# Optimization experiments

Measured on AMD Instinct MI355X. Metric: run time of the kernel, lower is better.

The kernel has to match this reference:

```python
import jax, jax.numpy as jnp
import numpy as np

EMBED_DIM = 768
NUM_HEADS = 12
HEAD_DIM = EMBED_DIM // NUM_HEADS


def setup_inputs() -> dict:
    key = jax.random.key(0)
    ks = jax.random.split(key, 5)
    B, N, D = 8, 1024, EMBED_DIM
    s = 1.0 / np.sqrt(D)
    return {
        "x": jax.random.normal(ks[0], (B, N, D), dtype=jnp.float32),
        "qkv_w": jax.random.uniform(ks[1], (D, 3 * D), jnp.float32, -s, s),  # [in, out]
        "qkv_b": jax.random.uniform(ks[2], (3 * D,), jnp.float32, -s, s),
        "proj_w": jax.random.uniform(ks[3], (D, D), jnp.float32, -s, s),
        "proj_b": jax.random.uniform(ks[4], (D,), jnp.float32, -s, s),
    }


def reference(x, qkv_w, qkv_b, proj_w, proj_b):
    B, N, D = x.shape
    H, Hd = NUM_HEADS, HEAD_DIM
    qkv = x @ qkv_w + qkv_b                          # [B, N, 3D]
    qkv = qkv.reshape(B, N, 3, H, Hd)
    q, k, v = (jnp.moveaxis(qkv, 2, 0)[i].transpose(0, 2, 1, 3) for i in range(3))  # each [B, H, N, Hd]
    scores = jnp.einsum("bhnd,bhmd->bhnm", q, k) / np.sqrt(Hd).astype(x.dtype)
    attn = jax.nn.softmax(scores, axis=-1)           # dropout rate 0.0 -> identity
    out = jnp.einsum("bhnm,bhmd->bhnd", attn, v)     # [B, H, N, Hd]
    out = out.transpose(0, 2, 1, 3).reshape(B, N, D)
    return out @ proj_w + proj_b
```

## Files before the change

### kernel.cpp

```cpp
#include <hip/hip_runtime.h>
#include <hip/hip_bf16.h>

typedef __attribute__((ext_vector_type(8))) short short8;
typedef __attribute__((ext_vector_type(4))) float f32x4;
typedef __attribute__((ext_vector_type(2))) unsigned int uint2v;
typedef unsigned int u32;

__device__ inline ushort f2bf(float f) {
    unsigned int i = __builtin_bit_cast(unsigned int, f);
    unsigned int r = (i + 0x7FFFu + ((i >> 16) & 1u)) >> 16;
    return (ushort)r;
}
__device__ inline u32 pack_bf16(float a, float b) {
    return (u32)f2bf(a) | ((u32)f2bf(b) << 16);
}

__device__ __forceinline__ void gload_lds16(const ushort* g, ushort* l) {
    __builtin_amdgcn_global_load_lds(
        (const __attribute__((address_space(1))) u32*)g,
        (__attribute__((address_space(3))) u32*)l, 16, 0, 0);
}

__global__ __launch_bounds__(256) void convert_f32_bf16(
    const float* __restrict__ in, ushort* __restrict__ outp, int n8)
{
    int idx = blockIdx.x * 256 + threadIdx.x;
    if (idx >= n8) return;
    const float4 u0 = *(const float4*)&in[(size_t)idx * 8];
    const float4 u1 = *(const float4*)&in[(size_t)idx * 8 + 4];
    short8 v;
    v[0] = (short)f2bf(u0.x); v[1] = (short)f2bf(u0.y);
    v[2] = (short)f2bf(u0.z); v[3] = (short)f2bf(u0.w);
    v[4] = (short)f2bf(u1.x); v[5] = (short)f2bf(u1.y);
    v[6] = (short)f2bf(u1.z); v[7] = (short)f2bf(u1.w);
    *(short8*)&outp[(size_t)idx * 8] = v;
}

__global__ __launch_bounds__(256) void transpose_f32_bf16(
    const float* __restrict__ W, ushort* __restrict__ Wt, int K, int N)
{
    __shared__ float tile[32][33];
    const int n0 = blockIdx.x * 32;
    const int k0 = blockIdx.y * 32;
    const int tx = threadIdx.x & 31;
    const int ty = threadIdx.x >> 5;
    for (int i = ty; i < 32; i += 8)
        tile[i][tx] = W[(size_t)(k0 + i) * N + n0 + tx];
    __syncthreads();
    for (int i = ty; i < 32; i += 8)
        Wt[(size_t)(n0 + i) * K + k0 + tx] = f2bf(tile[tx][i]);
}

template <bool OUT_FP32, bool QKV_MODE>
__global__ __launch_bounds__(256) void gemm_bt(
    const ushort* __restrict__ A, const ushort* __restrict__ Bt,
    const float* __restrict__ bias, void* __restrict__ C,
    ushort* __restrict__ Vt, int M, int N, int K, int ldc)
{
    __shared__ __attribute__((aligned(16))) ushort As[128][64];
    __shared__ __attribute__((aligned(16))) ushort Bs[128][64];
    const int tid  = threadIdx.x;
    const int lane = tid & 63;
    const int w    = tid >> 6;
    const int wm   = (w >> 1) * 64;
    const int wn   = (w & 1) * 64;
    const int g    = lane >> 4;
    const int t    = lane & 15;
    const int m0   = blockIdx.y * 128;
    const int n0   = blockIdx.x * 128;

    const int lr = lane >> 3;
    const int pc = lane & 7;

    f32x4 acc[4][4];
#pragma unroll
    for (int i = 0; i < 4; i++)
#pragma unroll
        for (int j = 0; j < 4; j++) acc[i][j] = {0.f, 0.f, 0.f, 0.f};

    const int xorc = t & 7;

    for (int k0 = 0; k0 < K; k0 += 64) {
#pragma unroll
        for (int p = 0; p < 4; p++) {
            const int row = w * 32 + p * 8 + lr;
            const int gc  = pc ^ (row & 7);
            gload_lds16(&A[(size_t)(m0 + row) * K + k0 + gc * 8], &As[w * 32 + p * 8][0]);
            gload_lds16(&Bt[(size_t)(n0 + row) * K + k0 + gc * 8], &Bs[w * 32 + p * 8][0]);
        }
        __syncthreads();
#pragma unroll
        for (int s = 0; s < 2; s++) {
            short8 a[4], b[4];
            const int ca = ((s * 4 + g) ^ xorc) * 8;
#pragma unroll
            for (int i = 0; i < 4; i++)
                a[i] = *(const short8*)&As[wm + i * 16 + t][ca];
#pragma unroll
            for (int j = 0; j < 4; j++)
                b[j] = *(const short8*)&Bs[wn + j * 16 + t][ca];
#pragma unroll
            for (int i = 0; i < 4; i++)
#pragma unroll
                for (int j = 0; j < 4; j++)
                    acc[i][j] = __builtin_amdgcn_mfma_f32_16x16x32_bf16(
                        a[i], b[j], acc[i][j], 0, 0, 0);
        }
        __syncthreads();
    }

#pragma unroll
    for (int j = 0; j < 4; j++) {
        int col = n0 + wn + j * 16 + t;
        float bv = bias[col];
        if (QKV_MODE && col >= 1536) {
            int h = (col - 1536) >> 6, d = col & 63;
#pragma unroll
            for (int i = 0; i < 4; i++) {
                int n = m0 + wm + i * 16 + g * 4;
                int bb = n >> 10, nn = n & 1023;
                uint2v u;
                u.x = pack_bf16(acc[i][j][0] + bv, acc[i][j][1] + bv);
                u.y = pack_bf16(acc[i][j][2] + bv, acc[i][j][3] + bv);
                *(uint2v*)&Vt[(((size_t)bb * 12 + h) * 64 + d) * 1024 + nn] = u;
            }
        } else {
#pragma unroll
            for (int i = 0; i < 4; i++)
#pragma unroll
                for (int r = 0; r < 4; r++) {
                    int row = m0 + wm + i * 16 + g * 4 + r;
                    float val = acc[i][j][r] + bv;
                    if (OUT_FP32) ((float*)C)[(size_t)row * ldc + col] = val;
                    else          ((ushort*)C)[(size_t)row * ldc + col] = f2bf(val);
                }
        }
    }
}

#define SD 72
__global__ __launch_bounds__(256) void attn_kernel(
    const ushort* __restrict__ qk, const ushort* __restrict__ Vt,
    ushort* __restrict__ out)
{
    __shared__ __attribute__((aligned(16))) ushort Ks[2][64][SD];
    __shared__ __attribute__((aligned(16))) ushort Vs[2][64][SD];
    __shared__ __attribute__((aligned(16))) ushort Ps[4][16][SD];

    const int tid  = threadIdx.x;
    const int lane = tid & 63;
    const int w    = tid >> 6;
    const int g    = lane >> 4;
    const int t    = lane & 15;
    const int q0   = blockIdx.x * 64;
    const int h    = blockIdx.y;
    const int b    = blockIdx.z;

    const int srow = tid >> 3;
    const int scol = (tid & 7) * 8;
    const size_t base  = (size_t)b * 1024 * 1536;
    const size_t vbase = ((size_t)b * 12 + h) * 64 * 1024;
    const float SC = 0.125f * 1.44269504088896f;

    short8 qfrag[2];
#pragma unroll
    for (int s = 0; s < 2; s++)
        qfrag[s] = *(const short8*)&qk[base + (size_t)(q0 + w * 16 + t) * 1536 +
                                       h * 64 + s * 32 + g * 8];

#pragma unroll
    for (int p = 0; p < 2; p++) {
        int r = srow + 32 * p;
        *(short8*)&Ks[0][r][scol] =
            *(const short8*)&qk[base + (size_t)r * 1536 + 768 + h * 64 + scol];
        *(short8*)&Vs[0][r][scol] =
            *(const short8*)&Vt[vbase + (size_t)r * 1024 + scol];
    }
    __syncthreads();

    f32x4 o_acc[4];
#pragma unroll
    for (int j = 0; j < 4; j++) o_acc[j] = {0.f, 0.f, 0.f, 0.f};
    float l_part = 0.f;

    for (int kt = 0; kt < 16; kt++) {
        const int cur = kt & 1;

        short8 kpre[2], vpre[2];
        if (kt < 15) {
            const int kb = (kt + 1) * 64;
#pragma unroll
            for (int p = 0; p < 2; p++) {
                int r = srow + 32 * p;
                kpre[p] = *(const short8*)&qk[base + (size_t)(kb + r) * 1536 + 768 + h * 64 + scol];
                vpre[p] = *(const short8*)&Vt[vbase + (size_t)r * 1024 + kb + scol];
            }
        }

        f32x4 s_acc[4];
#pragma unroll
        for (int j = 0; j < 4; j++) s_acc[j] = {0.f, 0.f, 0.f, 0.f};
#pragma unroll
        for (int s = 0; s < 2; s++)
#pragma unroll
            for (int j = 0; j < 4; j++) {
                short8 kf = *(const short8*)&Ks[cur][j * 16 + t][s * 32 + g * 8];
                s_acc[j] = __builtin_amdgcn_mfma_f32_16x16x32_bf16(kf, qfrag[s], s_acc[j], 0, 0, 0);
            }

#pragma unroll
        for (int j = 0; j < 4; j++) {
            float p0 = exp2f(s_acc[j][0] * SC);
            float p1 = exp2f(s_acc[j][1] * SC);
            float p2 = exp2f(s_acc[j][2] * SC);
            float p3 = exp2f(s_acc[j][3] * SC);
            l_part += (p0 + p1) + (p2 + p3);
            uint2v u;
            u.x = pack_bf16(p0, p1);
            u.y = pack_bf16(p2, p3);
            *(uint2v*)&Ps[w][t][j * 16 + g * 4] = u;
        }

#pragma unroll
        for (int s = 0; s < 2; s++) {
            short8 a = *(const short8*)&Ps[w][t][s * 32 + g * 8];
#pragma unroll
            for (int j = 0; j < 4; j++) {
                short8 bv = *(const short8*)&Vs[cur][j * 16 + t][s * 32 + g * 8];
                o_acc[j] = __builtin_amdgcn_mfma_f32_16x16x32_bf16(a, bv, o_acc[j], 0, 0, 0);
            }
        }

        if (kt < 15) {
#pragma unroll
            for (int p = 0; p < 2; p++) {
                int r = srow + 32 * p;
                *(short8*)&Ks[cur ^ 1][r][scol] = kpre[p];
                *(short8*)&Vs[cur ^ 1][r][scol] = vpre[p];
            }
        }
        __syncthreads();
    }

    float l_tot = l_part;
    l_tot += __shfl_xor(l_tot, 16);
    l_tot += __shfl_xor(l_tot, 32);
    float il[4];
#pragma unroll
    for (int r = 0; r < 4; r++) il[r] = 1.0f / __shfl(l_tot, g * 4 + r);
#pragma unroll
    for (int r = 0; r < 4; r++) {
        int row = q0 + w * 16 + g * 4 + r;
#pragma unroll
        for (int j = 0; j < 4; j++)
            out[((size_t)(b * 1024 + row)) * 768 + h * 64 + j * 16 + t] =
                f2bf(o_acc[j][r] * il[r]);
    }
}

extern "C" void kernel_launch(void* const* d_in, const int* in_sizes, int n_in,
                              void* d_out, int out_size, void* d_ws, size_t ws_size,
                              hipStream_t stream)
{
    const float* x      = (const float*)d_in[0];
    const float* qkv_w  = (const float*)d_in[1];
    const float* qkv_b  = (const float*)d_in[2];
    const float* proj_w = (const float*)d_in[3];
    const float* proj_b = (const float*)d_in[4];
    float* out = (float*)d_out;

    char* ws = (char*)d_ws;
    ushort* Wt1 = (ushort*)ws;
    ushort* Wt2 = Wt1 + (size_t)2304 * 768;
    char*   buf = (char*)(Wt2 + (size_t)768 * 768);

    transpose_f32_bf16<<<dim3(72, 24), 256, 0, stream>>>(qkv_w, Wt1, 768, 2304);
    transpose_f32_bf16<<<dim3(24, 24), 256, 0, stream>>>(proj_w, Wt2, 768, 768);

    const size_t wt_bytes   = ((size_t)2304 * 768 + (size_t)768 * 768) * 2;
    const size_t full_bytes = wt_bytes + (size_t)8192 * 768 * 2
                                       + (size_t)8192 * 1536 * 2
                                       + (size_t)8192 * 768 * 2
                                       + (size_t)8192 * 768 * 2;

    if (ws_size >= full_bytes) {
        ushort* xb    = (ushort*)buf;
        ushort* qkO   = xb + (size_t)8192 * 768;
        ushort* VtO   = qkO + (size_t)8192 * 1536;
        ushort* attnO = VtO + (size_t)8192 * 768;
        convert_f32_bf16<<<dim3(3072), 256, 0, stream>>>(x, xb, 786432);
        gemm_bt<false, true><<<dim3(18, 64), 256, 0, stream>>>(
            xb, Wt1, qkv_b, qkO, VtO, 8192, 2304, 768, 1536);
        attn_kernel<<<dim3(16, 12, 8), 256, 0, stream>>>(qkO, VtO, attnO);
        gemm_bt<true, false><<<dim3(6, 64), 256, 0, stream>>>(
            attnO, Wt2, proj_b, out, nullptr, 8192, 768, 768, 768);
    } else {
        ushort* xbB   = (ushort*)buf;
        ushort* qkB   = xbB + (size_t)1024 * 768;
        ushort* VtB   = qkB + (size_t)1024 * 1536;
        ushort* attnB = VtB + (size_t)1024 * 768;
        for (int b = 0; b < 8; b++) {
            const float* xp = x + (size_t)b * 1024 * 768;
            float* outb = out + (size_t)b * 1024 * 768;
            convert_f32_bf16<<<dim3(384), 256, 0, stream>>>(xp, xbB, 98304);
            gemm_bt<false, true><<<dim3(18, 8), 256, 0, stream>>>(
                xbB, Wt1, qkv_b, qkB, VtB, 1024, 2304, 768, 1536);
            attn_kernel<<<dim3(16, 12, 1), 256, 0, stream>>>(qkB, VtB, attnB);
            gemm_bt<true, false><<<dim3(6, 8), 256, 0, stream>>>(
                attnB, Wt2, proj_b, outb, nullptr, 1024, 768, 768, 768);
        }
    }
}
```

Before: 221.3 us.

## Process 128 queries per attention block with swizzled K/V LDS and prescaled Q

```diff
diff --git a/kernel.cpp b/kernel.cpp
--- a/kernel.cpp
+++ b/kernel.cpp
@@ -6,13 +6,18 @@
 typedef __attribute__((ext_vector_type(2))) unsigned int uint2v;
 typedef unsigned int u32;
 
+#define QSCALE 0.1803368801111204f
+
 __device__ inline ushort f2bf(float f) {
     unsigned int i = __builtin_bit_cast(unsigned int, f);
     unsigned int r = (i + 0x7FFFu + ((i >> 16) & 1u)) >> 16;
     return (ushort)r;
 }
 __device__ inline u32 pack_bf16(float a, float b) {
-    return (u32)f2bf(a) | ((u32)f2bf(b) << 16);
+    float2 f2; f2.x = a; f2.y = b;
+    __hip_bfloat162 h = __float22bfloat162_rn(f2);
+    u32 r; __builtin_memcpy(&r, &h, 4);
+    return r;
 }
 
 __device__ __forceinline__ void gload_lds16(const ushort* g, ushort* l) {
@@ -28,12 +33,11 @@
     if (idx >= n8) return;
     const float4 u0 = *(const float4*)&in[(size_t)idx * 8];
     const float4 u1 = *(const float4*)&in[(size_t)idx * 8 + 4];
-    short8 v;
-    v[0] = (short)f2bf(u0.x); v[1] = (short)f2bf(u0.y);
-    v[2] = (short)f2bf(u0.z); v[3] = (short)f2bf(u0.w);
-    v[4] = (short)f2bf(u1.x); v[5] = (short)f2bf(u1.y);
-    v[6] = (short)f2bf(u1.z); v[7] = (short)f2bf(u1.w);
-    *(short8*)&outp[(size_t)idx * 8] = v;
+    uint2v a, b;
+    a.x = pack_bf16(u0.x, u0.y); a.y = pack_bf16(u0.z, u0.w);
+    b.x = pack_bf16(u1.x, u1.y); b.y = pack_bf16(u1.z, u1.w);
+    *(uint2v*)&outp[(size_t)idx * 8] = a;
+    *(uint2v*)&outp[(size_t)idx * 8 + 4] = b;
 }
 
 __global__ __launch_bounds__(256) void transpose_f32_bf16(
@@ -131,6 +135,7 @@
                 for (int r = 0; r < 4; r++) {
                     int row = m0 + wm + i * 16 + g * 4 + r;
                     float val = acc[i][j][r] + bv;
+                    if (QKV_MODE && col < 768) val *= QSCALE;
                     if (OUT_FP32) ((float*)C)[(size_t)row * ldc + col] = val;
                     else          ((ushort*)C)[(size_t)row * ldc + col] = f2bf(val);
                 }
@@ -138,50 +143,54 @@
     }
 }
 
-#define SD 72
+#define PD 72
 __global__ __launch_bounds__(256) void attn_kernel(
     const ushort* __restrict__ qk, const ushort* __restrict__ Vt,
     ushort* __restrict__ out)
 {
-    __shared__ __attribute__((aligned(16))) ushort Ks[2][64][SD];
-    __shared__ __attribute__((aligned(16))) ushort Vs[2][64][SD];
-    __shared__ __attribute__((aligned(16))) ushort Ps[4][16][SD];
+    __shared__ __attribute__((aligned(16))) ushort Ks[2][64][64];
+    __shared__ __attribute__((aligned(16))) ushort Vs[2][64][64];
+    __shared__ __attribute__((aligned(16))) ushort Ps[4][16][PD];
 
     const int tid  = threadIdx.x;
     const int lane = tid & 63;
     const int w    = tid >> 6;
     const int g    = lane >> 4;
     const int t    = lane & 15;
-    const int q0   = blockIdx.x * 64;
+    const int q0   = blockIdx.x * 128;
     const int h    = blockIdx.y;
     const int b    = blockIdx.z;
 
     const int srow = tid >> 3;
-    const int scol = (tid & 7) * 8;
+    const int pc   = tid & 7;
     const size_t base  = (size_t)b * 1024 * 1536;
     const size_t vbase = ((size_t)b * 12 + h) * 64 * 1024;
-    const float SC = 0.125f * 1.44269504088896f;
-
-    short8 qfrag[2];
-#pragma unroll
-    for (int s = 0; s < 2; s++)
-        qfrag[s] = *(const short8*)&qk[base + (size_t)(q0 + w * 16 + t) * 1536 +
-                                       h * 64 + s * 32 + g * 8];
+
+    short8 qfrag[2][2];
+#pragma unroll
+    for (int qf = 0; qf < 2; qf++)
+#pragma unroll
+        for (int s = 0; s < 2; s++)
+            qfrag[qf][s] = *(const short8*)&qk[base +
+                (size_t)(q0 + qf * 64 + w * 16 + t) * 1536 + h * 64 + s * 32 + g * 8];
 
 #pragma unroll
     for (int p = 0; p < 2; p++) {
         int r = srow + 32 * p;
-        *(short8*)&Ks[0][r][scol] =
-            *(const short8*)&qk[base + (size_t)r * 1536 + 768 + h * 64 + scol];
-        *(short8*)&Vs[0][r][scol] =
-            *(const short8*)&Vt[vbase + (size_t)r * 1024 + scol];
+        int c = (pc ^ (r & 7)) * 8;
+        *(short8*)&Ks[0][r][c] =
+            *(const short8*)&qk[base + (size_t)r * 1536 + 768 + h * 64 + pc * 8];
+        *(short8*)&Vs[0][r][c] =
+            *(const short8*)&Vt[vbase + (size_t)r * 1024 + pc * 8];
     }
     __syncthreads();
 
-    f32x4 o_acc[4];
-#pragma unroll
-    for (int j = 0; j < 4; j++) o_acc[j] = {0.f, 0.f, 0.f, 0.f};
-    float l_part = 0.f;
+    f32x4 o_acc[2][4];
+#pragma unroll
+    for (int qf = 0; qf < 2; qf++)
+#pragma unroll
+        for (int j = 0; j < 4; j++) o_acc[qf][j] = {0.f, 0.f, 0.f, 0.f};
+    float l_part[2] = {0.f, 0.f};
 
     for (int kt = 0; kt < 16; kt++) {
         const int cur = kt & 1;
@@ -192,42 +201,54 @@
 #pragma unroll
             for (int p = 0; p < 2; p++) {
                 int r = srow + 32 * p;
-                kpre[p] = *(const short8*)&qk[base + (size_t)(kb + r) * 1536 + 768 + h * 64 + scol];
-                vpre[p] = *(const short8*)&Vt[vbase + (size_t)r * 1024 + kb + scol];
-            }
-        }
-
-        f32x4 s_acc[4];
-#pragma unroll
-        for (int j = 0; j < 4; j++) s_acc[j] = {0.f, 0.f, 0.f, 0.f};
+                kpre[p] = *(const short8*)&qk[base + (size_t)(kb + r) * 1536 + 768 + h * 64 + pc * 8];
+                vpre[p] = *(const short8*)&Vt[vbase + (size_t)r * 1024 + kb + pc * 8];
+            }
+        }
+
+        short8 kf[2][4], bv[2][4];
 #pragma unroll
         for (int s = 0; s < 2; s++)
 #pragma unroll
             for (int j = 0; j < 4; j++) {
-                short8 kf = *(const short8*)&Ks[cur][j * 16 + t][s * 32 + g * 8];
-                s_acc[j] = __builtin_amdgcn_mfma_f32_16x16x32_bf16(kf, qfrag[s], s_acc[j], 0, 0, 0);
-            }
-
-#pragma unroll
-        for (int j = 0; j < 4; j++) {
-            float p0 = exp2f(s_acc[j][0] * SC);
-            float p1 = exp2f(s_acc[j][1] * SC);
-            float p2 = exp2f(s_acc[j][2] * SC);
-            float p3 = exp2f(s_acc[j][3] * SC);
-            l_part += (p0 + p1) + (p2 + p3);
-            uint2v u;
-            u.x = pack_bf16(p0, p1);
-            u.y = pack_bf16(p2, p3);
-            *(uint2v*)&Ps[w][t][j * 16 + g * 4] = u;
-        }
-
-#pragma unroll
-        for (int s = 0; s < 2; s++) {
-            short8 a = *(const short8*)&Ps[w][t][s * 32 + g * 8];
+                const int row = j * 16 + t;
+                const int c = ((s * 4 + g) ^ (t & 7)) * 8;
+                kf[s][j] = *(const short8*)&Ks[cur][row][c];
+                bv[s][j] = *(const short8*)&Vs[cur][row][c];
+            }
+
+#pragma unroll
+        for (int qf = 0; qf < 2; qf++) {
+            f32x4 s_acc[4];
+#pragma unroll
+            for (int j = 0; j < 4; j++) s_acc[j] = {0.f, 0.f, 0.f, 0.f};
+#pragma unroll
+            for (int s = 0; s < 2; s++)
+#pragma unroll
+                for (int j = 0; j < 4; j++)
+                    s_acc[j] = __builtin_amdgcn_mfma_f32_16x16x32_bf16(
+                        kf[s][j], qfrag[qf][s], s_acc[j], 0, 0, 0);
+
 #pragma unroll
             for (int j = 0; j < 4; j++) {
-                short8 bv = *(const short8*)&Vs[cur][j * 16 + t][s * 32 + g * 8];
-                o_acc[j] = __builtin_amdgcn_mfma_f32_16x16x32_bf16(a, bv, o_acc[j], 0, 0, 0);
+                float p0 = exp2f(s_acc[j][0]);
+                float p1 = exp2f(s_acc[j][1]);
+                float p2 = exp2f(s_acc[j][2]);
+                float p3 = exp2f(s_acc[j][3]);
+                l_part[qf] += (p0 + p1) + (p2 + p3);
+                uint2v u;
+                u.x = pack_bf16(p0, p1);
+                u.y = pack_bf16(p2, p3);
+                *(uint2v*)&Ps[w][t][j * 16 + g * 4] = u;
+            }
+
+#pragma unroll
+            for (int s = 0; s < 2; s++) {
+                short8 a = *(const short8*)&Ps[w][t][s * 32 + g * 8];
+#pragma unroll
+                for (int j = 0; j < 4; j++)
+                    o_acc[qf][j] = __builtin_amdgcn_mfma_f32_16x16x32_bf16(
+                        a, bv[s][j], o_acc[qf][j], 0, 0, 0);
             }
         }
 
@@ -235,26 +256,30 @@
 #pragma unroll
             for (int p = 0; p < 2; p++) {
                 int r = srow + 32 * p;
-                *(short8*)&Ks[cur ^ 1][r][scol] = kpre[p];
-                *(short8*)&Vs[cur ^ 1][r][scol] = vpre[p];
+                int c = (pc ^ (r & 7)) * 8;
+                *(short8*)&Ks[cur ^ 1][r][c] = kpre[p];
+                *(short8*)&Vs[cur ^ 1][r][c] = vpre[p];
             }
         }
         __syncthreads();
     }
 
-    float l_tot = l_part;
-    l_tot += __shfl_xor(l_tot, 16);
-    l_tot += __shfl_xor(l_tot, 32);
-    float il[4];
-#pragma unroll
-    for (int r = 0; r < 4; r++) il[r] = 1.0f / __shfl(l_tot, g * 4 + r);
-#pragma unroll
-    for (int r = 0; r < 4; r++) {
-        int row = q0 + w * 16 + g * 4 + r;
-#pragma unroll
-        for (int j = 0; j < 4; j++)
-            out[((size_t)(b * 1024 + row)) * 768 + h * 64 + j * 16 + t] =
-                f2bf(o_acc[j][r] * il[r]);
+#pragma unroll
+    for (int qf = 0; qf < 2; qf++) {
+        float l_tot = l_part[qf];
+        l_tot += __shfl_xor(l_tot, 16);
+        l_tot += __shfl_xor(l_tot, 32);
+        float il[4];
+#pragma unroll
+        for (int r = 0; r < 4; r++) il[r] = 1.0f / __shfl(l_tot, g * 4 + r);
+#pragma unroll
+        for (int r = 0; r < 4; r++) {
+            int row = q0 + qf * 64 + w * 16 + g * 4 + r;
+#pragma unroll
+            for (int j = 0; j < 4; j++)
+                out[((size_t)(b * 1024 + row)) * 768 + h * 64 + j * 16 + t] =
+                    f2bf(o_acc[qf][j][r] * il[r]);
+        }
     }
 }
 
@@ -291,7 +316,7 @@
         convert_f32_bf16<<<dim3(3072), 256, 0, stream>>>(x, xb, 786432);
         gemm_bt<false, true><<<dim3(18, 64), 256, 0, stream>>>(
             xb, Wt1, qkv_b, qkO, VtO, 8192, 2304, 768, 1536);
-        attn_kernel<<<dim3(16, 12, 8), 256, 0, stream>>>(qkO, VtO, attnO);
+        attn_kernel<<<dim3(8, 12, 8), 256, 0, stream>>>(qkO, VtO, attnO);
         gemm_bt<true, false><<<dim3(6, 64), 256, 0, stream>>>(
             attnO, Wt2, proj_b, out, nullptr, 8192, 768, 768, 768);
     } else {
@@ -305,7 +330,7 @@
             convert_f32_bf16<<<dim3(384), 256, 0, stream>>>(xp, xbB, 98304);
             gemm_bt<false, true><<<dim3(18, 8), 256, 0, stream>>>(
                 xbB, Wt1, qkv_b, qkB, VtB, 1024, 2304, 768, 1536);
-            attn_kernel<<<dim3(16, 12, 1), 256, 0, stream>>>(qkB, VtB, attnB);
+            attn_kernel<<<dim3(8, 12, 1), 256, 0, stream>>>(qkB, VtB, attnB);
             gemm_bt<true, false><<<dim3(6, 8), 256, 0, stream>>>(
                 attnB, Wt2, proj_b, outb, nullptr, 1024, 768, 768, 768);
         }
```

Result: faster. 207.8 us (-6.1%).
